# Performance work log

Hardware: AMD Instinct MI355X
Metric: run time of the kernel (lower is better)

The kernel has to match this reference:

```python
import jax, jax.numpy as jnp
import numpy as np

N = 4096
F_IN = 512
F_OUT = 64
H = 8
ALPHA = 0.2
NEG_BIG = -9e15


def setup_inputs() -> dict:
    key = jax.random.key(0)
    ks = jax.random.split(key, 7)
    h = jax.random.normal(ks[0], (N, F_IN), dtype=jnp.float32)
    mask = jax.random.randint(ks[1], (N, N), 0, 2, dtype=jnp.int32)
    # per-head linear W: weight [H, F_IN, F_OUT], bias [H, F_OUT] (xavier-ish scale)
    w_scale = 1.414 * np.sqrt(6.0 / (F_IN + F_OUT))
    W = jax.random.uniform(ks[2], (H, F_IN, F_OUT), dtype=jnp.float32, minval=-w_scale, maxval=w_scale)
    bW = jnp.zeros((H, F_OUT), dtype=jnp.float32)
    # attention linear A: [2*F_OUT, 1] split into a_l (acts on Wh_i) and a_r (acts on Wh_j)
    a_scale = 1.414 * np.sqrt(6.0 / (2 * F_OUT + 1))
    a_l = jax.random.uniform(ks[3], (H, F_OUT), dtype=jnp.float32, minval=-a_scale, maxval=a_scale)
    a_r = jax.random.uniform(ks[4], (H, F_OUT), dtype=jnp.float32, minval=-a_scale, maxval=a_scale)
    bA = jnp.zeros((H,), dtype=jnp.float32)
    return {"h": h, "mask": mask, "W": W, "bW": bW, "a_l": a_l, "a_r": a_r, "bA": bA}


def reference(h, mask, W, bW, a_l, a_r, bA):
    # Wh: [H, N, F_OUT]
    Wh = jnp.einsum('ni,hio->hno', h, W) + bW[:, None, :]
    # A([Wh_i ; Wh_j]) decomposed as outer sum: e[h,i,j] = a_l.Wh_i + a_r.Wh_j + bA
    el = jnp.einsum('hno,ho->hn', Wh, a_l)  # [H, N]
    er = jnp.einsum('hno,ho->hn', Wh, a_r)  # [H, N]
    e = el[:, :, None] + er[:, None, :] + bA[:, None, None]  # [H, N, N]
    e = jax.nn.leaky_relu(e, negative_slope=ALPHA)
    e = jnp.where(mask[None] > 0, e, NEG_BIG)
    a = jax.nn.softmax(e, axis=-1)  # softmax over neighbors j (dim=1 in torch)
    # dropout omitted (eval mode / deterministic reference)
    aWh = jnp.einsum('hij,hjo->hio', a, Wh)  # [H, N, F_OUT]
    out = jax.nn.elu(aWh)  # last=False
    # concat heads along feature dim -> [N, H*F_OUT]
    return jnp.transpose(out, (1, 0, 2)).reshape(N, H * F_OUT)
```

## Files before the change

### kernel.cpp

```cpp
#include <hip/hip_runtime.h>
#include <hip/hip_bf16.h>

#define NN 4096
#define FIN 512
#define FOUT 64
#define NH 8
#define ALPHA 0.2f

typedef unsigned int uint;
typedef unsigned short ushort;
typedef unsigned char uchar;
typedef unsigned long long ull;
typedef __attribute__((ext_vector_type(8))) short short8;
typedef __attribute__((ext_vector_type(4))) float floatx4;

__device__ __forceinline__ float bf2f(ushort s) { return __uint_as_float(((uint)s) << 16); }
__device__ __forceinline__ ushort f2bf(float f) {
    uint u = __float_as_uint(f);
    u += 0x7fffu + ((u >> 16) & 1u);
    return (ushort)(u >> 16);
}

__device__ __forceinline__ int detect_bf16(const ushort* __restrict__ hraw) {
    int lane = threadIdx.x & 63;
    float a = fabsf(bf2f(hraw[2 * lane]));
    ull bal = __ballot(a >= 1e-3f && a <= 100.0f);
    return __popcll(bal) >= 32;
}

#define PM_BLKS 8192
#define CV_BLKS 1024
#define TW_BLKS 32

__global__ __launch_bounds__(256) void prep_kernel(
    const int* __restrict__ mask, uchar* __restrict__ mb,
    const void* __restrict__ hraw, ushort* __restrict__ bh,
    const void* __restrict__ Wraw, ushort* __restrict__ WT)
{
    const int b = blockIdx.x, t = threadIdx.x;
    if (b < PM_BLKS) {
        size_t gid = (size_t)b * 256 + t;
        const int* p = mask + gid * 8;
        int4 aa = *(const int4*)p;
        int4 bb = *(const int4*)(p + 4);
        uint by = (uint)(aa.x > 0)        | ((uint)(aa.y > 0) << 1)
                | ((uint)(aa.z > 0) << 2) | ((uint)(aa.w > 0) << 3)
                | ((uint)(bb.x > 0) << 4) | ((uint)(bb.y > 0) << 5)
                | ((uint)(bb.z > 0) << 6) | ((uint)(bb.w > 0) << 7);
        mb[gid] = (uchar)by;
    } else if (b < PM_BLKS + CV_BLKS) {
        int isbf = detect_bf16((const ushort*)hraw);
        size_t e0 = ((size_t)(b - PM_BLKS) * 256 + t) * 8;
        if (isbf) {
            *(uint4*)(bh + e0) = *(const uint4*)((const ushort*)hraw + e0);
        } else {
            const float* s = (const float*)hraw + e0;
            float4 f0 = *(const float4*)s;
            float4 f1 = *(const float4*)(s + 4);
            uint4 o;
            o.x = (uint)f2bf(f0.x) | ((uint)f2bf(f0.y) << 16);
            o.y = (uint)f2bf(f0.z) | ((uint)f2bf(f0.w) << 16);
            o.z = (uint)f2bf(f1.x) | ((uint)f2bf(f1.y) << 16);
            o.w = (uint)f2bf(f1.z) | ((uint)f2bf(f1.w) << 16);
            *(uint4*)(bh + e0) = o;
        }
    } else {
        int isbf = detect_bf16((const ushort*)hraw);
        int b2 = b - PM_BLKS - CV_BLKS;
        int h = b2 >> 2, kq = b2 & 3;
        int o = t & 63, sub = t >> 6;
        int kbase = kq * 128 + sub * 32;
        uint pk[16];
#pragma unroll
        for (int kk = 0; kk < 32; kk += 2) {
            float v0, v1;
            size_t s0 = ((size_t)h * FIN + kbase + kk) * FOUT + o;
            size_t s1 = s0 + FOUT;
            if (isbf) { v0 = bf2f(((const ushort*)Wraw)[s0]); v1 = bf2f(((const ushort*)Wraw)[s1]); }
            else      { v0 = ((const float*)Wraw)[s0];        v1 = ((const float*)Wraw)[s1]; }
            pk[kk >> 1] = (uint)f2bf(v0) | ((uint)f2bf(v1) << 16);
        }
        ushort* dst = WT + ((size_t)h * FOUT + o) * FIN + kbase;
#pragma unroll
        for (int q = 0; q < 4; q++)
            *(uint4*)(dst + q * 8) = make_uint4(pk[q*4], pk[q*4+1], pk[q*4+2], pk[q*4+3]);
    }
}

__global__ __launch_bounds__(256) void khv_kernel(const float* __restrict__ er,
                                                  float* __restrict__ Kh,
                                                  float* __restrict__ vt,
                                                  float* __restrict__ zt) {
    __shared__ float red[256];
    int h = blockIdx.x >> 3, sl = blockIdx.x & 7, t = threadIdx.x;
    float m = -3.0e38f;
    for (int j = t; j < NN; j += 256) m = fmaxf(m, er[(size_t)h * NN + j]);
    red[t] = m;
    __syncthreads();
    for (int s = 128; s >= 1; s >>= 1) {
        if (t < s) red[t] = fmaxf(red[t], red[t + s]);
        __syncthreads();
    }
    float kh = red[0];
    if (t == 0 && sl == 0) Kh[h] = kh;
    int j = sl * 512 + t;
#pragma unroll
    for (int q = 0; q < 2; q++, j += 256) {
        float d = er[(size_t)h * NN + j] - kh;
        vt[(size_t)h * NN + j] = __expf(d);
        zt[(size_t)h * NN + j] = __expf(ALPHA * d);
    }
}

__global__ __launch_bounds__(256) void wh_kernel(
    const ushort* __restrict__ hmat, const ushort* __restrict__ WT,
    const void* __restrict__ bWr, const void* __restrict__ alr,
    const void* __restrict__ arr, const void* __restrict__ bAr,
    const ushort* __restrict__ hraw,
    ushort* __restrict__ WhT, float* __restrict__ el, float* __restrict__ er)
{
    __shared__ __align__(16) ushort sT[64][72];
    const int t = threadIdx.x, lane = t & 63, wid = t >> 6;
    const int head = blockIdx.y, rbase = blockIdx.x * 64;
    const int lm = lane & 15, lq = lane >> 4;

    floatx4 C[4];
#pragma unroll
    for (int cg = 0; cg < 4; cg++) C[cg] = (floatx4){0.f, 0.f, 0.f, 0.f};

    const ushort* Ap = hmat + (size_t)(rbase + wid * 16 + lm) * FIN + lq * 8;
    const ushort* Bp = WT + (size_t)head * FOUT * FIN + (size_t)lm * FIN + lq * 8;

#pragma unroll
    for (int kc = 0; kc < 16; kc++) {
        short8 a = *(const short8*)(Ap + kc * 32);
#pragma unroll
        for (int cg = 0; cg < 4; cg++) {
            short8 b = *(const short8*)(Bp + (size_t)cg * 16 * FIN + kc * 32);
            C[cg] = __builtin_amdgcn_mfma_f32_16x16x32_bf16(a, b, C[cg], 0, 0, 0);
        }
    }

    const int isbf = detect_bf16(hraw);
    float bA = isbf ? bf2f(((const ushort*)bAr)[head]) : ((const float*)bAr)[head];
    float pel[4] = {0.f, 0.f, 0.f, 0.f}, per[4] = {0.f, 0.f, 0.f, 0.f};
#pragma unroll
    for (int cg = 0; cg < 4; cg++) {
        int o = head * FOUT + cg * 16 + lm;
        float bw = isbf ? bf2f(((const ushort*)bWr)[o]) : ((const float*)bWr)[o];
        float av = isbf ? bf2f(((const ushort*)alr)[o]) : ((const float*)alr)[o];
        float rv = isbf ? bf2f(((const ushort*)arr)[o]) : ((const float*)arr)[o];
        ushort pk[4];
#pragma unroll
        for (int r = 0; r < 4; r++) {
            float v = C[cg][r] + bw;
            pel[r] += v * av;
            per[r] += v * rv;
            pk[r] = f2bf(v);
        }
        ushort4 p4; p4.x = pk[0]; p4.y = pk[1]; p4.z = pk[2]; p4.w = pk[3];
        *(ushort4*)(&sT[cg * 16 + lm][wid * 16 + lq * 4]) = p4;
    }
#pragma unroll
    for (int off = 1; off < 16; off <<= 1) {
#pragma unroll
        for (int r = 0; r < 4; r++) {
            pel[r] += __shfl_xor(pel[r], off);
            per[r] += __shfl_xor(per[r], off);
        }
    }
    if (lm == 0) {
#pragma unroll
        for (int r = 0; r < 4; r++) {
            int row = rbase + wid * 16 + lq * 4 + r;
            el[(size_t)head * NN + row] = pel[r];
            er[(size_t)head * NN + row] = per[r] + bA;
        }
    }
    __syncthreads();
    {
        int o = t >> 2, ch = t & 3;
        uint4 v0 = *(const uint4*)(&sT[o][ch * 16]);
        uint4 v1 = *(const uint4*)(&sT[o][ch * 16 + 8]);
        ushort* d = WhT + ((size_t)head * FOUT + o) * NN + rbase + ch * 16;
        *(uint4*)d = v0;
        *(uint4*)(d + 8) = v1;
    }
}

__device__ __forceinline__ uint ppair(float v0, float v1, float z0, float z1,
                                      uint m2, float ui, float wi) {
    float p0 = fmaxf(ui * v0, wi * z0);
    float p1 = fmaxf(ui * v1, wi * z1);
    uint k0 = (uint)0 - (m2 & 1u);
    uint k1 = (uint)0 - ((m2 >> 1) & 1u);
    p0 = __uint_as_float(__float_as_uint(p0) & k0);
    p1 = __uint_as_float(__float_as_uint(p1) & k1);
    __hip_bfloat162 r = __float22bfloat162_rn(make_float2(p0, p1));
    return *(uint*)&r;
}

__device__ __forceinline__ short8 pgen8(float4 va, float4 vb, float4 za, float4 zb,
                                        uint mby, float ui, float wi) {
    union { uint4 u; short8 s; } c;
    c.u.x = ppair(va.x, va.y, za.x, za.y, mby,      ui, wi);
    c.u.y = ppair(va.z, va.w, za.z, za.w, mby >> 2, ui, wi);
    c.u.z = ppair(vb.x, vb.y, zb.x, zb.y, mby >> 4, ui, wi);
    c.u.w = ppair(vb.z, vb.w, zb.z, zb.w, mby >> 6, ui, wi);
    return c.s;
}

__global__ __launch_bounds__(256, 2) void attn_kernel(
    const uchar* __restrict__ mb,
    const ushort* __restrict__ WhT,
    const float* __restrict__ el, const float* __restrict__ Kh,
    const float* __restrict__ vt, const float* __restrict__ zt,
    const ushort* __restrict__ hraw,
    void* __restrict__ outv)
{
    __shared__ __align__(16) ushort sB[2][64 * 72];
    __shared__ float sv[2][64];
    __shared__ float sz[2][64];

    const int t = threadIdx.x, lane = t & 63, wid = t >> 6;
    const int b = blockIdx.x;
    const int head = b & 7;
    const int ibase = (b >> 3) * 64;
    const int lm = lane & 15, lq = lane >> 4;
    const int sh8 = lq * 8;

    const float kh = Kh[head];
    const float x = el[(size_t)head * NN + ibase + wid * 16 + lm] + kh;
    const float Mi = fmaxf(x, ALPHA * x);
    const float ui = __expf(x - Mi);
    const float wi = __expf(ALPHA * x - Mi);

    const int so = t >> 2;
    const int sc = (t & 3) * 16;
    const ushort* gB = WhT + ((size_t)head * FOUT + so) * NN + sc;
    const float* gvt = vt + (size_t)head * NN;
    const float* gzt = zt + (size_t)head * NN;
    const uchar* mrow = mb + (size_t)(ibase + wid * 16 + lm) * 512;

    uint4 r0, r1; float rvz = 0.f; uint2 mk_stage;

    auto gload = [&](int j0) {
        r0 = *(const uint4*)(gB + j0);
        r1 = *(const uint4*)(gB + j0 + 8);
        if (t < 128) rvz = (t < 64) ? gvt[j0 + t] : gzt[j0 + t - 64];
        mk_stage = *(const uint2*)(mrow + (j0 >> 3));
    };
    auto lwrite = [&](int buf) {
        *(uint4*)(&sB[buf][so * 72 + sc]) = r0;
        *(uint4*)(&sB[buf][so * 72 + sc + 8]) = r1;
        if (t < 128) { if (t < 64) sv[buf][t] = rvz; else sz[buf][t - 64] = rvz; }
    };

    const short8 ones = {0x3F80, 0x3F80, 0x3F80, 0x3F80, 0x3F80, 0x3F80, 0x3F80, 0x3F80};
    floatx4 C0 = {0.f, 0.f, 0.f, 0.f}, C1 = C0, C2 = C0, C3 = C0, Cd = C0;

    auto compute = [&](int buf, uint2 mk) {
        uint m0 = (mk.x >> sh8) & 0xFFu;
        uint m1 = (mk.y >> sh8) & 0xFFu;
        float4 va = *(const float4*)(&sv[buf][sh8]);
        float4 vb = *(const float4*)(&sv[buf][sh8 + 4]);
        float4 vc = *(const float4*)(&sv[buf][32 + sh8]);
        float4 vd = *(const float4*)(&sv[buf][36 + sh8]);
        float4 za = *(const float4*)(&sz[buf][sh8]);
        float4 zb = *(const float4*)(&sz[buf][sh8 + 4]);
        float4 zc = *(const float4*)(&sz[buf][32 + sh8]);
        float4 zd = *(const float4*)(&sz[buf][36 + sh8]);
        short8 a0 = pgen8(va, vb, za, zb, m0, ui, wi);
        short8 a1 = pgen8(vc, vd, zc, zd, m1, ui, wi);
        const ushort* base = &sB[buf][0];
        short8 b00 = *(const short8*)(base + (0  + lm) * 72 + sh8);
        short8 b10 = *(const short8*)(base + (16 + lm) * 72 + sh8);
        short8 b20 = *(const short8*)(base + (32 + lm) * 72 + sh8);
        short8 b30 = *(const short8*)(base + (48 + lm) * 72 + sh8);
        Cd = __builtin_amdgcn_mfma_f32_16x16x32_bf16(a0, ones, Cd, 0, 0, 0);
        C0 = __builtin_amdgcn_mfma_f32_16x16x32_bf16(a0, b00, C0, 0, 0, 0);
        C1 = __builtin_amdgcn_mfma_f32_16x16x32_bf16(a0, b10, C1, 0, 0, 0);
        C2 = __builtin_amdgcn_mfma_f32_16x16x32_bf16(a0, b20, C2, 0, 0, 0);
        C3 = __builtin_amdgcn_mfma_f32_16x16x32_bf16(a0, b30, C3, 0, 0, 0);
        short8 b01 = *(const short8*)(base + (0  + lm) * 72 + 32 + sh8);
        short8 b11 = *(const short8*)(base + (16 + lm) * 72 + 32 + sh8);
        short8 b21 = *(const short8*)(base + (32 + lm) * 72 + 32 + sh8);
        short8 b31 = *(const short8*)(base + (48 + lm) * 72 + 32 + sh8);
        Cd = __builtin_amdgcn_mfma_f32_16x16x32_bf16(a1, ones, Cd, 0, 0, 0);
        C0 = __builtin_amdgcn_mfma_f32_16x16x32_bf16(a1, b01, C0, 0, 0, 0);
        C1 = __builtin_amdgcn_mfma_f32_16x16x32_bf16(a1, b11, C1, 0, 0, 0);
        C2 = __builtin_amdgcn_mfma_f32_16x16x32_bf16(a1, b21, C2, 0, 0, 0);
        C3 = __builtin_amdgcn_mfma_f32_16x16x32_bf16(a1, b31, C3, 0, 0, 0);
    };

    gload(0);
    lwrite(0);
    uint2 mk0 = mk_stage;
    gload(64);
    __syncthreads();

    for (int it = 0; it < 64; it += 2) {
        compute(0, mk0);
        __syncthreads();
        lwrite(1);
        mk0 = mk_stage;
        gload(((it + 2) & 63) * 64);
        __syncthreads();
        compute(1, mk0);
        if (it < 62) {
            __syncthreads();
            lwrite(0);
            mk0 = mk_stage;
            gload(((it + 3) & 63) * 64);
            __syncthreads();
        }
    }

    const int isbf = detect_bf16(hraw);
#pragma unroll
    for (int r = 0; r < 4; r++) {
        int row = ibase + wid * 16 + lq * 4 + r;
        float inv = 1.f / Cd[r];
        float x0 = C0[r] * inv; x0 = (x0 > 0.f) ? x0 : __expf(x0) - 1.f;
        float x1 = C1[r] * inv; x1 = (x1 > 0.f) ? x1 : __expf(x1) - 1.f;
        float x2 = C2[r] * inv; x2 = (x2 > 0.f) ? x2 : __expf(x2) - 1.f;
        float x3 = C3[r] * inv; x3 = (x3 > 0.f) ? x3 : __expf(x3) - 1.f;
        size_t base = (size_t)row * (NH * FOUT) + head * FOUT + lm;
        if (isbf) {
            ushort* o = (ushort*)outv;
            o[base + 0]  = f2bf(x0);
            o[base + 16] = f2bf(x1);
            o[base + 32] = f2bf(x2);
            o[base + 48] = f2bf(x3);
        } else {
            float* o = (float*)outv;
            o[base + 0]  = x0;
            o[base + 16] = x1;
            o[base + 32] = x2;
            o[base + 48] = x3;
        }
    }
}

extern "C" void kernel_launch(void* const* d_in, const int* in_sizes, int n_in,
                              void* d_out, int out_size, void* d_ws, size_t ws_size,
                              hipStream_t stream)
{
    const void* hraw = d_in[0];
    const int*  mask = (const int*)d_in[1];
    const void* Wraw = d_in[2];
    const void* bWr  = d_in[3];
    const void* alr  = d_in[4];
    const void* arr  = d_in[5];
    const void* bAr  = d_in[6];

    char* w = (char*)d_ws;
    ushort* bh   = (ushort*)w;                  w += (size_t)NN * FIN * 2;
    ushort* WT   = (ushort*)w;                  w += (size_t)NH * FOUT * FIN * 2;
    ushort* WhT  = (ushort*)w;                  w += (size_t)NH * FOUT * NN * 2;
    float*  el   = (float*)w;                   w += (size_t)NH * NN * 4;
    float*  er   = (float*)w;                   w += (size_t)NH * NN * 4;
    float*  Kh   = (float*)w;                   w += 64;
    float*  vt   = (float*)w;                   w += (size_t)NH * NN * 4;
    float*  zt   = (float*)w;                   w += (size_t)NH * NN * 4;
    uchar*  mb   = (uchar*)w;                   w += (size_t)NN * 512;

    prep_kernel<<<PM_BLKS + CV_BLKS + TW_BLKS, 256, 0, stream>>>(
        mask, mb, hraw, bh, Wraw, WT);
    wh_kernel<<<dim3(NN / 64, NH), 256, 0, stream>>>(bh, WT, bWr, alr, arr, bAr,
                                                     (const ushort*)hraw, WhT, el, er);
    khv_kernel<<<64, 256, 0, stream>>>(er, Kh, vt, zt);
    attn_kernel<<<NN / 64 * NH, 256, 0, stream>>>(mb, WhT, el, Kh, vt, zt,
                                                  (const ushort*)hraw, d_out);
}
```

Measured before the change: 191.2 us.

## Give each attention wave two row tiles and load v/z directly into registers

The attention kernel now runs 2 waves per block instead of 4, and each wave computes 32 query rows (two 16-row MFMA tiles). That lets every B-fragment read from LDS feed twice as many MFMAs. The v/z score vectors are read straight from global memory into registers one stage ahead, replacing the shared-memory staging, and the loop is restructured to one barrier per stage. The trade-offs are fewer waves per block, doubled accumulator registers and lower occupancy, with more latency hiding left to the prefetch.

```diff
diff --git a/kernel.cpp b/kernel.cpp
--- a/kernel.cpp
+++ b/kernel.cpp
@@ -210,7 +210,18 @@
     return c.s;
 }
 
-__global__ __launch_bounds__(256, 2) void attn_kernel(
+#define VZLOAD(S, j0) do {                                      \
+    v##S##a = *(const float4*)(gvt + (j0) + sh8);               \
+    v##S##b = *(const float4*)(gvt + (j0) + sh8 + 4);           \
+    v##S##c = *(const float4*)(gvt + (j0) + 32 + sh8);          \
+    v##S##d = *(const float4*)(gvt + (j0) + 32 + sh8 + 4);      \
+    z##S##a = *(const float4*)(gzt + (j0) + sh8);               \
+    z##S##b = *(const float4*)(gzt + (j0) + sh8 + 4);           \
+    z##S##c = *(const float4*)(gzt + (j0) + 32 + sh8);          \
+    z##S##d = *(const float4*)(gzt + (j0) + 32 + sh8 + 4);      \
+} while (0)
+
+__global__ __launch_bounds__(128, 1) void attn_kernel(
     const uchar* __restrict__ mb,
     const ushort* __restrict__ WhT,
     const float* __restrict__ el, const float* __restrict__ Kh,
@@ -219,8 +230,6 @@
     void* __restrict__ outv)
 {
     __shared__ __align__(16) ushort sB[2][64 * 72];
-    __shared__ float sv[2][64];
-    __shared__ float sz[2][64];
 
     const int t = threadIdx.x, lane = t & 63, wid = t >> 6;
     const int b = blockIdx.x;
@@ -230,114 +239,151 @@
     const int sh8 = lq * 8;
 
     const float kh = Kh[head];
-    const float x = el[(size_t)head * NN + ibase + wid * 16 + lm] + kh;
-    const float Mi = fmaxf(x, ALPHA * x);
-    const float ui = __expf(x - Mi);
-    const float wi = __expf(ALPHA * x - Mi);
-
-    const int so = t >> 2;
-    const int sc = (t & 3) * 16;
+    const int rowa = ibase + wid * 32 + lm;
+    const float xa = el[(size_t)head * NN + rowa] + kh;
+    const float xb = el[(size_t)head * NN + rowa + 16] + kh;
+    const float Ma = fmaxf(xa, ALPHA * xa);
+    const float Mb = fmaxf(xb, ALPHA * xb);
+    const float uia = __expf(xa - Ma), wia = __expf(ALPHA * xa - Ma);
+    const float uib = __expf(xb - Mb), wib = __expf(ALPHA * xb - Mb);
+
+    const int so = t >> 1;
+    const int sc = (t & 1) * 32;
     const ushort* gB = WhT + ((size_t)head * FOUT + so) * NN + sc;
     const float* gvt = vt + (size_t)head * NN;
     const float* gzt = zt + (size_t)head * NN;
-    const uchar* mrow = mb + (size_t)(ibase + wid * 16 + lm) * 512;
-
-    uint4 r0, r1; float rvz = 0.f; uint2 mk_stage;
+    const uchar* mra = mb + (size_t)rowa * 512;
+    const uchar* mrb = mra + 16 * 512;
+
+    uint4 rr0, rr1, rr2, rr3;
+    uint2 mka_s, mkb_s;
 
     auto gload = [&](int j0) {
-        r0 = *(const uint4*)(gB + j0);
-        r1 = *(const uint4*)(gB + j0 + 8);
-        if (t < 128) rvz = (t < 64) ? gvt[j0 + t] : gzt[j0 + t - 64];
-        mk_stage = *(const uint2*)(mrow + (j0 >> 3));
+        rr0 = *(const uint4*)(gB + j0);
+        rr1 = *(const uint4*)(gB + j0 + 8);
+        rr2 = *(const uint4*)(gB + j0 + 16);
+        rr3 = *(const uint4*)(gB + j0 + 24);
+        mka_s = *(const uint2*)(mra + (j0 >> 3));
+        mkb_s = *(const uint2*)(mrb + (j0 >> 3));
     };
     auto lwrite = [&](int buf) {
-        *(uint4*)(&sB[buf][so * 72 + sc]) = r0;
-        *(uint4*)(&sB[buf][so * 72 + sc + 8]) = r1;
-        if (t < 128) { if (t < 64) sv[buf][t] = rvz; else sz[buf][t - 64] = rvz; }
+        ushort* d = &sB[buf][so * 72 + sc];
+        *(uint4*)(d)      = rr0;
+        *(uint4*)(d + 8)  = rr1;
+        *(uint4*)(d + 16) = rr2;
+        *(uint4*)(d + 24) = rr3;
     };
 
+    float4 v0a, v0b, v0c, v0d, z0a, z0b, z0c, z0d;
+    float4 v1a, v1b, v1c, v1d, z1a, z1b, z1c, z1d;
+
     const short8 ones = {0x3F80, 0x3F80, 0x3F80, 0x3F80, 0x3F80, 0x3F80, 0x3F80, 0x3F80};
-    floatx4 C0 = {0.f, 0.f, 0.f, 0.f}, C1 = C0, C2 = C0, C3 = C0, Cd = C0;
-
-    auto compute = [&](int buf, uint2 mk) {
-        uint m0 = (mk.x >> sh8) & 0xFFu;
-        uint m1 = (mk.y >> sh8) & 0xFFu;
-        float4 va = *(const float4*)(&sv[buf][sh8]);
-        float4 vb = *(const float4*)(&sv[buf][sh8 + 4]);
-        float4 vc = *(const float4*)(&sv[buf][32 + sh8]);
-        float4 vd = *(const float4*)(&sv[buf][36 + sh8]);
-        float4 za = *(const float4*)(&sz[buf][sh8]);
-        float4 zb = *(const float4*)(&sz[buf][sh8 + 4]);
-        float4 zc = *(const float4*)(&sz[buf][32 + sh8]);
-        float4 zd = *(const float4*)(&sz[buf][36 + sh8]);
-        short8 a0 = pgen8(va, vb, za, zb, m0, ui, wi);
-        short8 a1 = pgen8(vc, vd, zc, zd, m1, ui, wi);
+    floatx4 Z = {0.f, 0.f, 0.f, 0.f};
+    floatx4 C0 = Z, C1 = Z, C2 = Z, C3 = Z, Cd0 = Z;
+    floatx4 C4 = Z, C5 = Z, C6 = Z, C7 = Z, Cd1 = Z;
+
+    auto compute = [&](int buf, uint2 mka, uint2 mkb,
+                       float4 va, float4 vb, float4 vc, float4 vd,
+                       float4 za, float4 zb, float4 zc, float4 zd) {
+        uint m0a = (mka.x >> sh8) & 0xFFu;
+        uint m1a = (mka.y >> sh8) & 0xFFu;
+        uint m0b = (mkb.x >> sh8) & 0xFFu;
+        uint m1b = (mkb.y >> sh8) & 0xFFu;
+        short8 a0 = pgen8(va, vb, za, zb, m0a, uia, wia);
+        short8 a1 = pgen8(vc, vd, zc, zd, m1a, uia, wia);
+        short8 a2 = pgen8(va, vb, za, zb, m0b, uib, wib);
+        short8 a3 = pgen8(vc, vd, zc, zd, m1b, uib, wib);
         const ushort* base = &sB[buf][0];
         short8 b00 = *(const short8*)(base + (0  + lm) * 72 + sh8);
         short8 b10 = *(const short8*)(base + (16 + lm) * 72 + sh8);
         short8 b20 = *(const short8*)(base + (32 + lm) * 72 + sh8);
         short8 b30 = *(const short8*)(base + (48 + lm) * 72 + sh8);
-        Cd = __builtin_amdgcn_mfma_f32_16x16x32_bf16(a0, ones, Cd, 0, 0, 0);
+        Cd0 = __builtin_amdgcn_mfma_f32_16x16x32_bf16(a0, ones, Cd0, 0, 0, 0);
+        Cd1 = __builtin_amdgcn_mfma_f32_16x16x32_bf16(a2, ones, Cd1, 0, 0, 0);
         C0 = __builtin_amdgcn_mfma_f32_16x16x32_bf16(a0, b00, C0, 0, 0, 0);
+        C4 = __builtin_amdgcn_mfma_f32_16x16x32_bf16(a2, b00, C4, 0, 0, 0);
         C1 = __builtin_amdgcn_mfma_f32_16x16x32_bf16(a0, b10, C1, 0, 0, 0);
+        C5 = __builtin_amdgcn_mfma_f32_16x16x32_bf16(a2, b10, C5, 0, 0, 0);
         C2 = __builtin_amdgcn_mfma_f32_16x16x32_bf16(a0, b20, C2, 0, 0, 0);
+        C6 = __builtin_amdgcn_mfma_f32_16x16x32_bf16(a2, b20, C6, 0, 0, 0);
         C3 = __builtin_amdgcn_mfma_f32_16x16x32_bf16(a0, b30, C3, 0, 0, 0);
+        C7 = __builtin_amdgcn_mfma_f32_16x16x32_bf16(a2, b30, C7, 0, 0, 0);
         short8 b01 = *(const short8*)(base + (0  + lm) * 72 + 32 + sh8);
         short8 b11 = *(const short8*)(base + (16 + lm) * 72 + 32 + sh8);
         short8 b21 = *(const short8*)(base + (32 + lm) * 72 + 32 + sh8);
         short8 b31 = *(const short8*)(base + (48 + lm) * 72 + 32 + sh8);
-        Cd = __builtin_amdgcn_mfma_f32_16x16x32_bf16(a1, ones, Cd, 0, 0, 0);
+        Cd0 = __builtin_amdgcn_mfma_f32_16x16x32_bf16(a1, ones, Cd0, 0, 0, 0);
+        Cd1 = __builtin_amdgcn_mfma_f32_16x16x32_bf16(a3, ones, Cd1, 0, 0, 0);
         C0 = __builtin_amdgcn_mfma_f32_16x16x32_bf16(a1, b01, C0, 0, 0, 0);
+        C4 = __builtin_amdgcn_mfma_f32_16x16x32_bf16(a3, b01, C4, 0, 0, 0);
         C1 = __builtin_amdgcn_mfma_f32_16x16x32_bf16(a1, b11, C1, 0, 0, 0);
+        C5 = __builtin_amdgcn_mfma_f32_16x16x32_bf16(a3, b11, C5, 0, 0, 0);
         C2 = __builtin_amdgcn_mfma_f32_16x16x32_bf16(a1, b21, C2, 0, 0, 0);
+        C6 = __builtin_amdgcn_mfma_f32_16x16x32_bf16(a3, b21, C6, 0, 0, 0);
         C3 = __builtin_amdgcn_mfma_f32_16x16x32_bf16(a1, b31, C3, 0, 0, 0);
+        C7 = __builtin_amdgcn_mfma_f32_16x16x32_bf16(a3, b31, C7, 0, 0, 0);
     };
 
+    uint2 mka0, mkb0, mka1, mkb1;
     gload(0);
     lwrite(0);
-    uint2 mk0 = mk_stage;
+    mka0 = mka_s; mkb0 = mkb_s;
     gload(64);
+    VZLOAD(0, 0);
     __syncthreads();
 
     for (int it = 0; it < 64; it += 2) {
-        compute(0, mk0);
+        lwrite(1);
+        mka1 = mka_s; mkb1 = mkb_s;
+        gload(((it + 2) & 63) * 64);
+        VZLOAD(1, (it + 1) * 64);
+        compute(0, mka0, mkb0, v0a, v0b, v0c, v0d, z0a, z0b, z0c, z0d);
         __syncthreads();
-        lwrite(1);
-        mk0 = mk_stage;
-        gload(((it + 2) & 63) * 64);
+        lwrite(0);
+        mka0 = mka_s; mkb0 = mkb_s;
+        gload(((it + 3) & 63) * 64);
+        VZLOAD(0, ((it + 2) & 63) * 64);
+        compute(1, mka1, mkb1, v1a, v1b, v1c, v1d, z1a, z1b, z1c, z1d);
         __syncthreads();
-        compute(1, mk0);
-        if (it < 62) {
-            __syncthreads();
-            lwrite(0);
-            mk0 = mk_stage;
-            gload(((it + 3) & 63) * 64);
-            __syncthreads();
-        }
     }
 
     const int isbf = detect_bf16(hraw);
 #pragma unroll
     for (int r = 0; r < 4; r++) {
-        int row = ibase + wid * 16 + lq * 4 + r;
-        float inv = 1.f / Cd[r];
-        float x0 = C0[r] * inv; x0 = (x0 > 0.f) ? x0 : __expf(x0) - 1.f;
-        float x1 = C1[r] * inv; x1 = (x1 > 0.f) ? x1 : __expf(x1) - 1.f;
-        float x2 = C2[r] * inv; x2 = (x2 > 0.f) ? x2 : __expf(x2) - 1.f;
-        float x3 = C3[r] * inv; x3 = (x3 > 0.f) ? x3 : __expf(x3) - 1.f;
-        size_t base = (size_t)row * (NH * FOUT) + head * FOUT + lm;
+        int ra = ibase + wid * 32 + lq * 4 + r;
+        int rb = ra + 16;
+        float inva = 1.f / Cd0[r];
+        float invb = 1.f / Cd1[r];
+        float x0 = C0[r] * inva; x0 = (x0 > 0.f) ? x0 : __expf(x0) - 1.f;
+        float x1 = C1[r] * inva; x1 = (x1 > 0.f) ? x1 : __expf(x1) - 1.f;
+        float x2 = C2[r] * inva; x2 = (x2 > 0.f) ? x2 : __expf(x2) - 1.f;
+        float x3 = C3[r] * inva; x3 = (x3 > 0.f) ? x3 : __expf(x3) - 1.f;
+        float y0 = C4[r] * invb; y0 = (y0 > 0.f) ? y0 : __expf(y0) - 1.f;
+        float y1 = C5[r] * invb; y1 = (y1 > 0.f) ? y1 : __expf(y1) - 1.f;
+        float y2 = C6[r] * invb; y2 = (y2 > 0.f) ? y2 : __expf(y2) - 1.f;
+        float y3 = C7[r] * invb; y3 = (y3 > 0.f) ? y3 : __expf(y3) - 1.f;
+        size_t basea = (size_t)ra * (NH * FOUT) + head * FOUT + lm;
+        size_t baseb = (size_t)rb * (NH * FOUT) + head * FOUT + lm;
         if (isbf) {
             ushort* o = (ushort*)outv;
-            o[base + 0]  = f2bf(x0);
-            o[base + 16] = f2bf(x1);
-            o[base + 32] = f2bf(x2);
-            o[base + 48] = f2bf(x3);
+            o[basea + 0]  = f2bf(x0);
+            o[basea + 16] = f2bf(x1);
+            o[basea + 32] = f2bf(x2);
+            o[basea + 48] = f2bf(x3);
+            o[baseb + 0]  = f2bf(y0);
+            o[baseb + 16] = f2bf(y1);
+            o[baseb + 32] = f2bf(y2);
+            o[baseb + 48] = f2bf(y3);
         } else {
             float* o = (float*)outv;
-            o[base + 0]  = x0;
-            o[base + 16] = x1;
-            o[base + 32] = x2;
-            o[base + 48] = x3;
+            o[basea + 0]  = x0;
+            o[basea + 16] = x1;
+            o[basea + 32] = x2;
+            o[basea + 48] = x3;
+            o[baseb + 0]  = y0;
+            o[baseb + 16] = y1;
+            o[baseb + 32] = y2;
+            o[baseb + 48] = y3;
         }
     }
 }
@@ -370,6 +416,6 @@
     wh_kernel<<<dim3(NN / 64, NH), 256, 0, stream>>>(bh, WT, bWr, alr, arr, bAr,
                                                      (const ushort*)hraw, WhT, el, er);
     khv_kernel<<<64, 256, 0, stream>>>(er, Kh, vt, zt);
-    attn_kernel<<<NN / 64 * NH, 256, 0, stream>>>(mb, WhT, el, Kh, vt, zt,
+    attn_kernel<<<NN / 64 * NH, 128, 0, stream>>>(mb, WhT, el, Kh, vt, zt,
                                                   (const ushort*)hraw, d_out);
 }
```

New measurement: 205.0 us. 1.07x slower.

## Halve barriers per tile and load v/z attention terms directly into registers

Applied to the files above, without the earlier changes.

Reorders the double-buffered main loop so the next tile's shared-memory write and global prefetch are issued before the current tile's compute. This cuts the barriers from four to two per pair of tiles. The v/z per-column score terms no longer go through shared memory: each lane loads its needed float4 slices straight from global memory, one tile ahead, into a second register set. This removes the LDS staging and the extra barrier it needed, but adds redundant global and L1 loads per lane and raises register pressure under the two-blocks-per-CU launch bound.

```diff
diff --git a/kernel.cpp b/kernel.cpp
--- a/kernel.cpp
+++ b/kernel.cpp
@@ -210,6 +210,17 @@
     return c.s;
 }
 
+#define VZLOAD(S, j0) do {                                      \
+    v##S##a = *(const float4*)(gvt + (j0) + sh8);               \
+    v##S##b = *(const float4*)(gvt + (j0) + sh8 + 4);           \
+    v##S##c = *(const float4*)(gvt + (j0) + 32 + sh8);          \
+    v##S##d = *(const float4*)(gvt + (j0) + 32 + sh8 + 4);      \
+    z##S##a = *(const float4*)(gzt + (j0) + sh8);               \
+    z##S##b = *(const float4*)(gzt + (j0) + sh8 + 4);           \
+    z##S##c = *(const float4*)(gzt + (j0) + 32 + sh8);          \
+    z##S##d = *(const float4*)(gzt + (j0) + 32 + sh8 + 4);      \
+} while (0)
+
 __global__ __launch_bounds__(256, 2) void attn_kernel(
     const uchar* __restrict__ mb,
     const ushort* __restrict__ WhT,
@@ -219,8 +230,6 @@
     void* __restrict__ outv)
 {
     __shared__ __align__(16) ushort sB[2][64 * 72];
-    __shared__ float sv[2][64];
-    __shared__ float sz[2][64];
 
     const int t = threadIdx.x, lane = t & 63, wid = t >> 6;
     const int b = blockIdx.x;
@@ -230,7 +239,8 @@
     const int sh8 = lq * 8;
 
     const float kh = Kh[head];
-    const float x = el[(size_t)head * NN + ibase + wid * 16 + lm] + kh;
+    const int row = ibase + wid * 16 + lm;
+    const float x = el[(size_t)head * NN + row] + kh;
     const float Mi = fmaxf(x, ALPHA * x);
     const float ui = __expf(x - Mi);
     const float wi = __expf(ALPHA * x - Mi);
@@ -240,36 +250,34 @@
     const ushort* gB = WhT + ((size_t)head * FOUT + so) * NN + sc;
     const float* gvt = vt + (size_t)head * NN;
     const float* gzt = zt + (size_t)head * NN;
-    const uchar* mrow = mb + (size_t)(ibase + wid * 16 + lm) * 512;
-
-    uint4 r0, r1; float rvz = 0.f; uint2 mk_stage;
+    const uchar* mrow = mb + (size_t)row * 512;
+
+    uint4 rr0, rr1;
+    uint2 mk_s;
 
     auto gload = [&](int j0) {
-        r0 = *(const uint4*)(gB + j0);
-        r1 = *(const uint4*)(gB + j0 + 8);
-        if (t < 128) rvz = (t < 64) ? gvt[j0 + t] : gzt[j0 + t - 64];
-        mk_stage = *(const uint2*)(mrow + (j0 >> 3));
+        rr0 = *(const uint4*)(gB + j0);
+        rr1 = *(const uint4*)(gB + j0 + 8);
+        mk_s = *(const uint2*)(mrow + (j0 >> 3));
     };
     auto lwrite = [&](int buf) {
-        *(uint4*)(&sB[buf][so * 72 + sc]) = r0;
-        *(uint4*)(&sB[buf][so * 72 + sc + 8]) = r1;
-        if (t < 128) { if (t < 64) sv[buf][t] = rvz; else sz[buf][t - 64] = rvz; }
+        ushort* d = &sB[buf][so * 72 + sc];
+        *(uint4*)(d)     = rr0;
+        *(uint4*)(d + 8) = rr1;
     };
 
+    float4 v0a, v0b, v0c, v0d, z0a, z0b, z0c, z0d;
+    float4 v1a, v1b, v1c, v1d, z1a, z1b, z1c, z1d;
+
     const short8 ones = {0x3F80, 0x3F80, 0x3F80, 0x3F80, 0x3F80, 0x3F80, 0x3F80, 0x3F80};
-    floatx4 C0 = {0.f, 0.f, 0.f, 0.f}, C1 = C0, C2 = C0, C3 = C0, Cd = C0;
-
-    auto compute = [&](int buf, uint2 mk) {
+    floatx4 Z = {0.f, 0.f, 0.f, 0.f};
+    floatx4 C0 = Z, C1 = Z, C2 = Z, C3 = Z, Cd = Z;
+
+    auto compute = [&](int buf, uint2 mk,
+                       float4 va, float4 vb, float4 vc, float4 vd,
+                       float4 za, float4 zb, float4 zc, float4 zd) {
         uint m0 = (mk.x >> sh8) & 0xFFu;
         uint m1 = (mk.y >> sh8) & 0xFFu;
-        float4 va = *(const float4*)(&sv[buf][sh8]);
-        float4 vb = *(const float4*)(&sv[buf][sh8 + 4]);
-        float4 vc = *(const float4*)(&sv[buf][32 + sh8]);
-        float4 vd = *(const float4*)(&sv[buf][36 + sh8]);
-        float4 za = *(const float4*)(&sz[buf][sh8]);
-        float4 zb = *(const float4*)(&sz[buf][sh8 + 4]);
-        float4 zc = *(const float4*)(&sz[buf][32 + sh8]);
-        float4 zd = *(const float4*)(&sz[buf][36 + sh8]);
         short8 a0 = pgen8(va, vb, za, zb, m0, ui, wi);
         short8 a1 = pgen8(vc, vd, zc, zd, m1, ui, wi);
         const ushort* base = &sB[buf][0];
@@ -293,39 +301,39 @@
         C3 = __builtin_amdgcn_mfma_f32_16x16x32_bf16(a1, b31, C3, 0, 0, 0);
     };
 
+    uint2 mk0, mk1;
     gload(0);
     lwrite(0);
-    uint2 mk0 = mk_stage;
+    mk0 = mk_s;
     gload(64);
+    VZLOAD(0, 0);
     __syncthreads();
 
     for (int it = 0; it < 64; it += 2) {
-        compute(0, mk0);
+        lwrite(1);
+        mk1 = mk_s;
+        gload(((it + 2) & 63) * 64);
+        VZLOAD(1, (it + 1) * 64);
+        compute(0, mk0, v0a, v0b, v0c, v0d, z0a, z0b, z0c, z0d);
         __syncthreads();
-        lwrite(1);
-        mk0 = mk_stage;
-        gload(((it + 2) & 63) * 64);
+        lwrite(0);
+        mk0 = mk_s;
+        gload(((it + 3) & 63) * 64);
+        VZLOAD(0, ((it + 2) & 63) * 64);
+        compute(1, mk1, v1a, v1b, v1c, v1d, z1a, z1b, z1c, z1d);
         __syncthreads();
-        compute(1, mk0);
-        if (it < 62) {
-            __syncthreads();
-            lwrite(0);
-            mk0 = mk_stage;
-            gload(((it + 3) & 63) * 64);
-            __syncthreads();
-        }
     }
 
     const int isbf = detect_bf16(hraw);
 #pragma unroll
     for (int r = 0; r < 4; r++) {
-        int row = ibase + wid * 16 + lq * 4 + r;
+        int orow = ibase + wid * 16 + lq * 4 + r;
         float inv = 1.f / Cd[r];
         float x0 = C0[r] * inv; x0 = (x0 > 0.f) ? x0 : __expf(x0) - 1.f;
         float x1 = C1[r] * inv; x1 = (x1 > 0.f) ? x1 : __expf(x1) - 1.f;
         float x2 = C2[r] * inv; x2 = (x2 > 0.f) ? x2 : __expf(x2) - 1.f;
         float x3 = C3[r] * inv; x3 = (x3 > 0.f) ? x3 : __expf(x3) - 1.f;
-        size_t base = (size_t)row * (NH * FOUT) + head * FOUT + lm;
+        size_t base = (size_t)orow * (NH * FOUT) + head * FOUT + lm;
         if (isbf) {
             ushort* o = (ushort*)outv;
             o[base + 0]  = f2bf(x0);
```

Measured after the change: 190.1 us. Within noise of the previous version (-0.6%).
